# Kernel tuning notes

Measured on AMD Instinct MI355X. Metric: run time of the kernel, lower is better.

## Reference

```python
import jax, jax.numpy as jnp
import numpy as np

NX, NY, C, B, P = 432, 496, 64, 4, 40000


def setup_inputs() -> dict:
    key = jax.random.key(0)
    k1, _ = jax.random.split(key)
    pillar_features = jax.random.normal(k1, (P, C), dtype=jnp.float32)
    # Build voxel_coords with unique (x, y) cells per batch element so the
    # scatter-write has no duplicate indices (matches deterministic torch assignment).
    rng = np.random.default_rng(0)
    per = P // B  # pillars per sample
    coords = np.empty((P, 3), dtype=np.int64)
    for b in range(B):
        flat = rng.choice(NX * NY, size=per, replace=False)
        coords[b * per:(b + 1) * per, 0] = flat % NX          # x index
        coords[b * per:(b + 1) * per, 1] = flat // NX         # y index
        coords[b * per:(b + 1) * per, 2] = b                  # batch index (last col)
    return {
        "pillar_features": pillar_features,
        "voxel_coords": jnp.asarray(coords),
        "batch_size": B,
        "nx": NX,
        "ny": NY,
    }


def reference(pillar_features, voxel_coords, batch_size, nx, ny):
    # Fused scatter: compute a global flat index (batch, y, x) for every pillar
    # and scatter all pillars in a single pass (no per-batch masking loop).
    x = voxel_coords[:, 0]
    y = voxel_coords[:, 1]
    b = voxel_coords[:, -1]
    flat = b * (ny * nx) + y * nx + x                       # [P]
    c = pillar_features.shape[1]
    grid = jnp.zeros((batch_size * ny * nx, c), dtype=pillar_features.dtype)
    grid = grid.at[flat].set(pillar_features)               # scatter pillars
    # [B*ny*nx, C] -> [B, C, ny, nx]
    return grid.reshape(batch_size, ny, nx, c).transpose(0, 3, 1, 2)
```

## Files before the change

### kernel.cpp

```cpp
#include <hip/hip_runtime.h>


#define C_CH 64

__global__ void build_map_kernel(const int* __restrict__ coords, int n_pillars,
                                 const int* __restrict__ nx_p,
                                 const int* __restrict__ ny_p,
                                 int* __restrict__ map) {
    int p = blockIdx.x * blockDim.x + threadIdx.x;
    if (p >= n_pillars) return;
    const int nx = nx_p[0];
    const int ny = ny_p[0];
    const int x = coords[3 * p + 0];
    const int y = coords[3 * p + 1];
    const int b = coords[3 * p + 2];
    const long long m = (long long)b * (long long)(nx * ny) + (long long)y * nx + x;
    map[m] = p;
}

__global__ void gather64_kernel(const float* __restrict__ feat,
                                const int* __restrict__ map,
                                const int* __restrict__ nx_p,
                                const int* __restrict__ ny_p,
                                float* __restrict__ out, int n_map) {
    const int tid = blockIdx.x * blockDim.x + threadIdx.x;
    if (tid >= n_map) return;
    const int plane = nx_p[0] * ny_p[0];
    const int b = tid / plane;
    const int rem = tid - b * plane;
    const size_t base = (size_t)b * C_CH * (size_t)plane + (size_t)rem;

    const int p = map[tid];

    float vals[C_CH];
#pragma unroll
    for (int c = 0; c < C_CH; ++c) vals[c] = 0.0f;

    if (p >= 0) {
        const float4* __restrict__ src =
            (const float4*)(feat + (size_t)p * C_CH);
#pragma unroll
        for (int i = 0; i < C_CH / 4; ++i) {
            float4 v = src[i];
            vals[4 * i + 0] = v.x;
            vals[4 * i + 1] = v.y;
            vals[4 * i + 2] = v.z;
            vals[4 * i + 3] = v.w;
        }
    }

#pragma unroll
    for (int c = 0; c < C_CH; ++c) {
        out[base + (size_t)c * (size_t)plane] = vals[c];
    }
}

__global__ void direct_scatter_kernel(const float* __restrict__ feat,
                                      const int* __restrict__ coords,
                                      int n_pillars, int C,
                                      const int* __restrict__ nx_p,
                                      const int* __restrict__ ny_p,
                                      float* __restrict__ out) {
    const long long t = (long long)blockIdx.x * blockDim.x + threadIdx.x;
    if (t >= (long long)n_pillars * C) return;
    const int p = (int)(t / C);
    const int c = (int)(t - (long long)p * C);
    const int nx = nx_p[0];
    const int ny = ny_p[0];
    const int x = coords[3 * p + 0];
    const int y = coords[3 * p + 1];
    const int b = coords[3 * p + 2];
    const int plane = nx * ny;
    const size_t o = ((size_t)b * C + c) * (size_t)plane + (size_t)y * nx + x;
    out[o] = feat[(size_t)p * C + c];
}

extern "C" void kernel_launch(void* const* d_in, const int* in_sizes, int n_in,
                              void* d_out, int out_size, void* d_ws, size_t ws_size,
                              hipStream_t stream) {
    const float* feat   = (const float*)d_in[0];
    const int*   coords = (const int*)d_in[1];
    const int* nx_p = (const int*)d_in[3];
    const int* ny_p = (const int*)d_in[4];
    float* out = (float*)d_out;

    const int n_pillars = in_sizes[1] / 3;
    const int C = in_sizes[0] / n_pillars;
    const int n_map = out_size / C;
    const size_t map_bytes = (size_t)n_map * sizeof(int);

    if (C == C_CH && ws_size >= map_bytes) {
        int* map = (int*)d_ws;
        hipMemsetAsync(map, 0xFF, map_bytes, stream);
        build_map_kernel<<<(n_pillars + 255) / 256, 256, 0, stream>>>(
            coords, n_pillars, nx_p, ny_p, map);
        gather64_kernel<<<(n_map + 255) / 256, 256, 0, stream>>>(
            feat, map, nx_p, ny_p, out, n_map);
    } else {
        hipMemsetAsync(out, 0, (size_t)out_size * sizeof(float), stream);
        const long long total = (long long)n_pillars * C;
        direct_scatter_kernel<<<(unsigned)((total + 255) / 256), 256, 0, stream>>>(
            feat, coords, n_pillars, C, nx_p, ny_p, out);
    }
}
```

Measured before the change: 232.7 us.

## Gather into slices with shared-memory transposed features and vectorized stores

Replaces the one-thread-per-cell gather with one block per slice of 3348 grid cells. The block first compacts the occupied cells of its slice into a slot list. It then loads those pillars' feature rows with coalesced reads into a transposed shared-memory tile. Each thread then writes four adjacent cells per channel as a float4 store. This targets the scattered 256-byte per-thread feature reads and the scalar output stores of the old kernel. The cost is a fixed slice size tied to the plane size, a capacity limit that sends overflow pillars to slow global reads, and only one large block per slice, which lowers the number of blocks in flight.

```diff
diff --git a/kernel.cpp b/kernel.cpp
--- a/kernel.cpp
+++ b/kernel.cpp
@@ -1,7 +1,12 @@
 #include <hip/hip_runtime.h>
 
 
-#define C_CH 64
+#define C_CH   64
+#define SLICE  3348
+#define CAP    216
+#define BT     1024
+
+typedef float fvec4 __attribute__((ext_vector_type(4)));
 
 __global__ void build_map_kernel(const int* __restrict__ coords, int n_pillars,
                                  const int* __restrict__ nx_p,
@@ -18,40 +23,89 @@
     map[m] = p;
 }
 
-__global__ void gather64_kernel(const float* __restrict__ feat,
-                                const int* __restrict__ map,
-                                const int* __restrict__ nx_p,
-                                const int* __restrict__ ny_p,
-                                float* __restrict__ out, int n_map) {
-    const int tid = blockIdx.x * blockDim.x + threadIdx.x;
-    if (tid >= n_map) return;
+__global__ __launch_bounds__(BT) void gather_slice_kernel(
+    const float* __restrict__ feat, const int* __restrict__ map,
+    const int* __restrict__ nx_p, const int* __restrict__ ny_p,
+    float* __restrict__ out, int n_map) {
+    __shared__ float featT[C_CH][CAP];
+    __shared__ __align__(16) unsigned short slot_of[SLICE + 4];
+    __shared__ int pil[CAP];
+    __shared__ int cnt;
+
+    const int T = threadIdx.x;
+    if (T == 0) cnt = 0;
+    __syncthreads();
+
+    const int cell0 = blockIdx.x * SLICE;
+    const int len = min(SLICE, n_map - cell0);
     const int plane = nx_p[0] * ny_p[0];
-    const int b = tid / plane;
-    const int rem = tid - b * plane;
-    const size_t base = (size_t)b * C_CH * (size_t)plane + (size_t)rem;
 
-    const int p = map[tid];
+    for (int i = T; i < SLICE + 4; i += BT) {
+        unsigned short s = 0xFFFFu;
+        if (i < len) {
+            const int p = map[cell0 + i];
+            if (p >= 0) {
+                const int k = atomicAdd(&cnt, 1);
+                if (k < CAP) { pil[k] = p; s = (unsigned short)k; }
+                else s = 0xFFFEu;
+            }
+        }
+        slot_of[i] = s;
+    }
+    __syncthreads();
 
-    float vals[C_CH];
+    const int total = min(cnt, CAP);
+    for (int idx = T; idx < total * C_CH; idx += BT) {
+        const int s = idx >> 6;
+        const int e = idx & 63;
+        featT[e][s] = feat[(size_t)pil[s] * C_CH + e];
+    }
+    __syncthreads();
+
+    const int b0 = cell0 / plane;
+    const int bend = (cell0 + len - 1) / plane;
+    const int local0 = cell0 - b0 * plane;
+    const bool fast = (b0 == bend) && ((plane & 3) == 0) &&
+                      ((local0 & 3) == 0) && ((len & 3) == 0);
+
+    if (fast) {
+        const int q = T;
+        const int nq = len >> 2;
+        if (q < nq) {
+            const ushort4 sl = *reinterpret_cast<const ushort4*>(&slot_of[4 * q]);
+            const unsigned short ss[4] = {sl.x, sl.y, sl.z, sl.w};
+            fvec4* dst = (fvec4*)(out + (size_t)(b0 * C_CH) * (size_t)plane +
+                                  local0 + 4 * q);
+            const int pstep = plane >> 2;
+#pragma unroll 4
+            for (int c = 0; c < C_CH; ++c) {
+                float vv[4];
 #pragma unroll
-    for (int c = 0; c < C_CH; ++c) vals[c] = 0.0f;
-
-    if (p >= 0) {
-        const float4* __restrict__ src =
-            (const float4*)(feat + (size_t)p * C_CH);
-#pragma unroll
-        for (int i = 0; i < C_CH / 4; ++i) {
-            float4 v = src[i];
-            vals[4 * i + 0] = v.x;
-            vals[4 * i + 1] = v.y;
-            vals[4 * i + 2] = v.z;
-            vals[4 * i + 3] = v.w;
+                for (int j = 0; j < 4; ++j) {
+                    const unsigned short s = ss[j];
+                    float f = 0.0f;
+                    if (s < CAP) f = featT[c][s];
+                    else if (s == 0xFFFEu)
+                        f = feat[(size_t)map[cell0 + 4 * q + j] * C_CH + c];
+                    vv[j] = f;
+                }
+                fvec4 v;
+                v.x = vv[0]; v.y = vv[1]; v.z = vv[2]; v.w = vv[3];
+                *dst = v;
+                dst += pstep;
+            }
         }
-    }
-
-#pragma unroll
-    for (int c = 0; c < C_CH; ++c) {
-        out[base + (size_t)c * (size_t)plane] = vals[c];
+    } else {
+        for (int i = T; i < len; i += BT) {
+            const int cell = cell0 + i;
+            const int b = cell / plane;
+            const int local = cell - b * plane;
+            const int p = map[cell];
+            for (int c = 0; c < C_CH; ++c) {
+                out[((size_t)(b * C_CH + c)) * (size_t)plane + local] =
+                    (p >= 0) ? feat[(size_t)p * C_CH + c] : 0.0f;
+            }
+        }
     }
 }
 
@@ -91,13 +145,15 @@
 
     if (C == C_CH && ws_size >= map_bytes) {
         int* map = (int*)d_ws;
-        hipMemsetAsync(map, 0xFF, map_bytes, stream);
+        (void)hipMemsetAsync(map, 0xFF, map_bytes, stream);
         build_map_kernel<<<(n_pillars + 255) / 256, 256, 0, stream>>>(
             coords, n_pillars, nx_p, ny_p, map);
-        gather64_kernel<<<(n_map + 255) / 256, 256, 0, stream>>>(
+
+        const int n_blocks = (n_map + SLICE - 1) / SLICE;
+        gather_slice_kernel<<<n_blocks, BT, 0, stream>>>(
             feat, map, nx_p, ny_p, out, n_map);
     } else {
-        hipMemsetAsync(out, 0, (size_t)out_size * sizeof(float), stream);
+        (void)hipMemsetAsync(out, 0, (size_t)out_size * sizeof(float), stream);
         const long long total = (long long)n_pillars * C;
         direct_scatter_kernel<<<(unsigned)((total + 255) / 256), 256, 0, stream>>>(
             feat, coords, n_pillars, C, nx_p, ny_p, out);
```

Result: no change. 236.7 us (+1.7%).
